# Performance work log

Measured on AMD Instinct MI355X. Metric: run time of the kernel, lower is better.

The kernel has to match this reference:

```python
import jax, jax.numpy as jnp
import numpy as np

B, K, H, E = 4096, 8, 4096, 64

def setup_inputs() -> dict:
    key = jax.random.key(0)
    k1, k2, k3, k4 = jax.random.split(key, 4)
    x = jax.random.normal(k1, (B, H), dtype=jnp.float32)
    expert_ids = jax.random.randint(k2, (B, K), 0, E, dtype=jnp.int32)
    expert_scales = jax.random.uniform(k3, (B, K), dtype=jnp.float32)
    golden_expand_x = jax.random.normal(k4, (B * K, H), dtype=jnp.float32)
    return {"x": x, "expert_ids": expert_ids, "expert_scales": expert_scales,
            "golden_expand_x": golden_expand_x, "moe_expert_num": E}


def reference(x, expert_ids, expert_scales, golden_expand_x, moe_expert_num):
    # --- dispatch: group token-expert pairs by expert id (stable sort) ---
    b, k = expert_ids.shape
    flat_e = expert_ids.reshape(-1)                      # [B*K]
    order = jnp.argsort(flat_e, stable=True)             # dispatch permutation
    # dispatched activations (what the NPU op would gather); overridden below
    # by golden_expand_x, mirroring is_cascade_golden_expand_x=True.
    expand_x = x[order // k]                              # [B*K, H]
    expand_x = golden_expand_x                            # golden override
    # assist_info_for_combine: position of each (token, k) slot in expand_x
    inv = jnp.argsort(order)                              # [B*K]
    # --- combine: gather each slot back and reduce with routing scales ---
    gathered = expand_x[inv].reshape(b, k, -1)            # [B, K, H]
    out = jnp.einsum('bk,bkh->bh', expert_scales, gathered)  # [B, H]
    # loop output is iteration-invariant: x_combine_res == last combine out
    return (out, out)
```

## Files before the change

### kernel.cpp

```cpp
#include <hip/hip_runtime.h>

#define B_TOK 4096
#define K_EXP 8
#define H_DIM 4096
#define E_NUM 64
#define N_SLOT (B_TOK * K_EXP)
#define NBLK 64
#define CHUNK 512

__global__ void hist_kernel(const int* __restrict__ eids, int* __restrict__ part) {
    __shared__ int cnt[E_NUM];
    const int tid = threadIdx.x;
    if (tid < E_NUM) cnt[tid] = 0;
    __syncthreads();
    const int i = blockIdx.x * CHUNK + tid;
    const int e = eids[i];
    atomicAdd(&cnt[e], 1);
    __syncthreads();
    if (tid < E_NUM) part[blockIdx.x * E_NUM + tid] = cnt[tid];
}

__global__ void scan_kernel(const int* __restrict__ part, int* __restrict__ offs) {
    __shared__ int totals[E_NUM];
    const int e = threadIdx.x;
    int tot = 0;
    for (int b = 0; b < NBLK; ++b) tot += part[b * E_NUM + e];
    totals[e] = tot;
    __syncthreads();
    int base = 0;
    for (int ee = 0; ee < e; ++ee) base += totals[ee];
    int run = base;
    for (int b = 0; b < NBLK; ++b) {
        offs[b * E_NUM + e] = run;
        run += part[b * E_NUM + e];
    }
}

__global__ void inv_kernel(const int* __restrict__ eids, const int* __restrict__ offs,
                           int* __restrict__ inv) {
    __shared__ unsigned char ids[CHUNK];
    const int tid = threadIdx.x;
    const int i = blockIdx.x * CHUNK + tid;
    const int e = eids[i];
    ids[tid] = (unsigned char)e;
    __syncthreads();
    int rank = 0;
    for (int j = 0; j < tid; ++j) rank += (ids[j] == (unsigned char)e) ? 1 : 0;
    inv[i] = offs[blockIdx.x * E_NUM + e] + rank;
}

__global__ __launch_bounds__(256) void combine_kernel(
        const float* __restrict__ scales,
        const float* __restrict__ ex,
        const int* __restrict__ inv,
        float* __restrict__ out0,
        float* __restrict__ out1) {
    const int b = blockIdx.x;
    __shared__ int   rows[K_EXP];
    __shared__ float ss[K_EXP];
    const int tid = threadIdx.x;
    if (tid < K_EXP) {
        rows[tid] = inv[b * K_EXP + tid];
        ss[tid]   = scales[b * K_EXP + tid];
    }
    __syncthreads();

    const float4* ex4 = (const float4*)ex;
    float4* o0 = (float4*)(out0 + (size_t)b * H_DIM);
    float4* o1 = (float4*)(out1 + (size_t)b * H_DIM);
    const int H4 = H_DIM / 4;

    size_t rbase[K_EXP];
    float  sreg[K_EXP];
#pragma unroll
    for (int k = 0; k < K_EXP; ++k) {
        rbase[k] = (size_t)rows[k] * H4;
        sreg[k]  = ss[k];
    }

#pragma unroll
    for (int it = 0; it < 4; ++it) {
        const int c = tid + it * 256;
        float4 acc = make_float4(0.f, 0.f, 0.f, 0.f);
#pragma unroll
        for (int k = 0; k < K_EXP; ++k) {
            const float4 v = ex4[rbase[k] + c];
            const float s = sreg[k];
            acc.x += s * v.x; acc.y += s * v.y;
            acc.z += s * v.z; acc.w += s * v.w;
        }
        o0[c] = acc;
        o1[c] = acc;
    }
}

extern "C" void kernel_launch(void* const* d_in, const int* in_sizes, int n_in,
                              void* d_out, int out_size, void* d_ws, size_t ws_size,
                              hipStream_t stream) {
    const int*   eids   = (const int*)d_in[1];
    const float* scales = (const float*)d_in[2];
    const float* ex     = (const float*)d_in[3];
    float* out0 = (float*)d_out;
    float* out1 = (float*)d_out + (size_t)B_TOK * H_DIM;

    int* ws   = (int*)d_ws;
    int* part = ws;
    int* offs = ws + NBLK * E_NUM;
    int* inv  = ws + 2 * NBLK * E_NUM;

    hist_kernel<<<NBLK, CHUNK, 0, stream>>>(eids, part);
    scan_kernel<<<1, E_NUM, 0, stream>>>(part, offs);
    inv_kernel<<<NBLK, CHUNK, 0, stream>>>(eids, offs, inv);
    combine_kernel<<<B_TOK, 256, 0, stream>>>(scales, ex, inv, out0, out1);
}
```

Measured before the change: 775.8 us.

## Fuse dispatch ranking into combine kernel via per-block ballot counting

Drops the histogram, scan and inverse-permutation kernels. Each combine block now computes the stable-sort rank of its 8 slots by scanning all 32K expert ids, comparing packed (expert<<15|index) keys with wave ballots. Loads from the expanded activations and the output stores become nontemporal. This saves three launches and their serial dependency, but every block redundantly reads the full id array (128KB) and does a large number of ballot operations, which could cost more than it saves.

```diff
diff --git a/kernel.cpp b/kernel.cpp
--- a/kernel.cpp
+++ b/kernel.cpp
@@ -5,69 +5,65 @@
 #define H_DIM 4096
 #define E_NUM 64
 #define N_SLOT (B_TOK * K_EXP)
-#define NBLK 64
-#define CHUNK 512
 
-__global__ void hist_kernel(const int* __restrict__ eids, int* __restrict__ part) {
-    __shared__ int cnt[E_NUM];
-    const int tid = threadIdx.x;
-    if (tid < E_NUM) cnt[tid] = 0;
-    __syncthreads();
-    const int i = blockIdx.x * CHUNK + tid;
-    const int e = eids[i];
-    atomicAdd(&cnt[e], 1);
-    __syncthreads();
-    if (tid < E_NUM) part[blockIdx.x * E_NUM + tid] = cnt[tid];
-}
+typedef float vf4 __attribute__((ext_vector_type(4)));
 
-__global__ void scan_kernel(const int* __restrict__ part, int* __restrict__ offs) {
-    __shared__ int totals[E_NUM];
-    const int e = threadIdx.x;
-    int tot = 0;
-    for (int b = 0; b < NBLK; ++b) tot += part[b * E_NUM + e];
-    totals[e] = tot;
-    __syncthreads();
-    int base = 0;
-    for (int ee = 0; ee < e; ++ee) base += totals[ee];
-    int run = base;
-    for (int b = 0; b < NBLK; ++b) {
-        offs[b * E_NUM + e] = run;
-        run += part[b * E_NUM + e];
-    }
-}
-
-__global__ void inv_kernel(const int* __restrict__ eids, const int* __restrict__ offs,
-                           int* __restrict__ inv) {
-    __shared__ unsigned char ids[CHUNK];
-    const int tid = threadIdx.x;
-    const int i = blockIdx.x * CHUNK + tid;
-    const int e = eids[i];
-    ids[tid] = (unsigned char)e;
-    __syncthreads();
-    int rank = 0;
-    for (int j = 0; j < tid; ++j) rank += (ids[j] == (unsigned char)e) ? 1 : 0;
-    inv[i] = offs[blockIdx.x * E_NUM + e] + rank;
-}
-
-__global__ __launch_bounds__(256) void combine_kernel(
+__global__ __launch_bounds__(256) void moe_fused(
+        const int*   __restrict__ eids,
         const float* __restrict__ scales,
         const float* __restrict__ ex,
-        const int* __restrict__ inv,
         float* __restrict__ out0,
         float* __restrict__ out1) {
-    const int b = blockIdx.x;
+    const int b    = blockIdx.x;
+    const int tid  = threadIdx.x;
+    const int lane = tid & 63;
+    const int wid  = tid >> 6;
+
+    unsigned kk[K_EXP];
+#pragma unroll
+    for (int k = 0; k < K_EXP; ++k) {
+        const int i = b * K_EXP + k;
+        kk[k] = ((unsigned)eids[i] << 15) | (unsigned)i;
+    }
+
+    int cnt[K_EXP];
+#pragma unroll
+    for (int k = 0; k < K_EXP; ++k) cnt[k] = 0;
+
+    const int4* e4 = (const int4*)eids;
+    for (int s = 0; s < N_SLOT / 4 / 256; ++s) {
+        const int idx = s * 256 + tid;
+        const int4 v  = e4[idx];
+        const unsigned j0 = (unsigned)idx * 4u;
+        const unsigned kj0 = ((unsigned)v.x << 15) | (j0 + 0u);
+        const unsigned kj1 = ((unsigned)v.y << 15) | (j0 + 1u);
+        const unsigned kj2 = ((unsigned)v.z << 15) | (j0 + 2u);
+        const unsigned kj3 = ((unsigned)v.w << 15) | (j0 + 3u);
+#pragma unroll
+        for (int k = 0; k < K_EXP; ++k) {
+            cnt[k] += __popcll(__ballot(kj0 < kk[k]));
+            cnt[k] += __popcll(__ballot(kj1 < kk[k]));
+            cnt[k] += __popcll(__ballot(kj2 < kk[k]));
+            cnt[k] += __popcll(__ballot(kj3 < kk[k]));
+        }
+    }
+    __shared__ int   red[4][K_EXP];
     __shared__ int   rows[K_EXP];
     __shared__ float ss[K_EXP];
-    const int tid = threadIdx.x;
+    if (lane == 0) {
+#pragma unroll
+        for (int k = 0; k < K_EXP; ++k) red[wid][k] = cnt[k];
+    }
+    __syncthreads();
     if (tid < K_EXP) {
-        rows[tid] = inv[b * K_EXP + tid];
+        rows[tid] = red[0][tid] + red[1][tid] + red[2][tid] + red[3][tid];
         ss[tid]   = scales[b * K_EXP + tid];
     }
     __syncthreads();
 
-    const float4* ex4 = (const float4*)ex;
-    float4* o0 = (float4*)(out0 + (size_t)b * H_DIM);
-    float4* o1 = (float4*)(out1 + (size_t)b * H_DIM);
+    const vf4* ex4 = (const vf4*)ex;
+    vf4* o0 = (vf4*)(out0 + (size_t)b * H_DIM);
+    vf4* o1 = (vf4*)(out1 + (size_t)b * H_DIM);
     const int H4 = H_DIM / 4;
 
     size_t rbase[K_EXP];
@@ -81,35 +77,26 @@
 #pragma unroll
     for (int it = 0; it < 4; ++it) {
         const int c = tid + it * 256;
-        float4 acc = make_float4(0.f, 0.f, 0.f, 0.f);
+        vf4 acc = (vf4)0.0f;
 #pragma unroll
         for (int k = 0; k < K_EXP; ++k) {
-            const float4 v = ex4[rbase[k] + c];
-            const float s = sreg[k];
-            acc.x += s * v.x; acc.y += s * v.y;
-            acc.z += s * v.z; acc.w += s * v.w;
+            const vf4 v = __builtin_nontemporal_load(&ex4[rbase[k] + c]);
+            acc += v * sreg[k];
         }
-        o0[c] = acc;
-        o1[c] = acc;
+        __builtin_nontemporal_store(acc, &o0[c]);
+        __builtin_nontemporal_store(acc, &o1[c]);
     }
 }
 
 extern "C" void kernel_launch(void* const* d_in, const int* in_sizes, int n_in,
                               void* d_out, int out_size, void* d_ws, size_t ws_size,
                               hipStream_t stream) {
+    (void)d_ws; (void)ws_size;
     const int*   eids   = (const int*)d_in[1];
     const float* scales = (const float*)d_in[2];
     const float* ex     = (const float*)d_in[3];
     float* out0 = (float*)d_out;
     float* out1 = (float*)d_out + (size_t)B_TOK * H_DIM;
 
-    int* ws   = (int*)d_ws;
-    int* part = ws;
-    int* offs = ws + NBLK * E_NUM;
-    int* inv  = ws + 2 * NBLK * E_NUM;
-
-    hist_kernel<<<NBLK, CHUNK, 0, stream>>>(eids, part);
-    scan_kernel<<<1, E_NUM, 0, stream>>>(part, offs);
-    inv_kernel<<<NBLK, CHUNK, 0, stream>>>(eids, offs, inv);
-    combine_kernel<<<B_TOK, 256, 0, stream>>>(scales, ex, inv, out0, out1);
+    moe_fused<<<B_TOK, 256, 0, stream>>>(eids, scales, ex, out0, out1);
 }
```

Result: faster. 744.2 us (-4.1%).
